# Kernel optimization log

Hardware: AMD Instinct MI355X
Metric: run time of the kernel (lower is better)

Reference implementation:

```python
import jax, jax.numpy as jnp
from jax import lax
import numpy as np

B, N, H, T, NPB = 1024, 50, 128, 50, 3
C_TANH, NEG = 10.0, 1e9


def _lstm(x, h, c, Wi, Wh, b):
    gates = x @ Wi + h @ Wh + b
    i, f, g, o = jnp.split(gates, 4, axis=-1)
    c2 = jax.nn.sigmoid(f) * c + jax.nn.sigmoid(i) * jnp.tanh(g)
    return jax.nn.sigmoid(o) * jnp.tanh(c2), c2


def setup_inputs() -> dict:
    key = jax.random.key(0)
    ks = jax.random.split(key, 20)
    rn = lambda k, shape, fan: (jax.random.normal(k, shape, jnp.float32) / np.float32(np.sqrt(fan)))
    return {
        'input_pnt': jax.random.uniform(ks[0], (B, N, 2), jnp.float32),
        'W_emb': rn(ks[1], (2, H), 2), 'b_emb': jnp.zeros((H,), jnp.float32),
        'dec_init': rn(ks[2], (1, 1, H), H),
        'Wi': rn(ks[3], (H, 4 * H), H), 'Wh': rn(ks[4], (H, 4 * H), H), 'b_lstm': jnp.zeros((4 * H,), jnp.float32),
        'Wq_g': rn(ks[5], (H, H), H), 'Wref_g': rn(ks[6], (H, H), H), 'v_g': rn(ks[7], (H,), H),
        'Wq_p': rn(ks[8], (H, H), H), 'Wref_p': rn(ks[9], (H, H), H), 'v_p': rn(ks[10], (H,), H),
        'Wi_c': rn(ks[11], (H, 4 * H), H), 'Wh_c': rn(ks[12], (H, 4 * H), H), 'b_c': jnp.zeros((4 * H,), jnp.float32),
        'Wq_c': rn(ks[13], (H, H), H), 'Wref_c': rn(ks[14], (H, H), H), 'v_c': rn(ks[15], (H,), H),
        'W1': rn(ks[16], (H, H), H), 'b1': jnp.zeros((H,), jnp.float32),
        'W2': rn(ks[17], (H, 1), H), 'b2': jnp.zeros((1,), jnp.float32),
    }


def _forward(input_pnt, W_emb, b_emb, dec_init, Wi, Wh, b_lstm, Wq_g, Wref_g, v_g,
             Wq_p, Wref_p, v_p, Wi_c, Wh_c, b_c, Wq_c, Wref_c, v_c, W1, b1, W2, b2):
    context = input_pnt @ W_emb + b_emb                    # [B,N,H] embedded nodes
    e_g = context @ Wref_g                                  # glimpse keys (step-invariant, hoisted)
    e_p = context @ Wref_p                                  # pointer keys (hoisted)
    z = jnp.zeros((B, H), context.dtype)
    carry0 = (z, z, jnp.zeros((B, N), context.dtype), jnp.broadcast_to(dec_init[0, 0], (B, H)))

    def step(carry, _):
        h, c, mask, dec_in = carry
        h2, c2 = _lstm(dec_in, h, c, Wi, Wh, b_lstm)
        # glimpse attention (masked)
        q = h2 @ Wq_g
        u = jnp.einsum('bnh,h->bn', jnp.tanh(e_g + q[:, None, :]), v_g) - NEG * mask
        g = jnp.einsum('bn,bnh->bh', jax.nn.softmax(u, -1), e_g)
        # pointer attention with tanh exploration clipping (masked)
        u2 = jnp.einsum('bnh,h->bn', jnp.tanh(e_p + (g @ Wq_p)[:, None, :]), v_p)
        logit = C_TANH * jnp.tanh(u2) - NEG * mask
        logprob = jax.nn.log_softmax(logit, -1)
        prob = jax.nn.softmax(logit, -1)
        action = jnp.argmax(prob, -1)                       # greedy decode
        mask2 = jnp.maximum(mask, jax.nn.one_hot(action, N, dtype=mask.dtype))
        dec_next = jnp.take_along_axis(context, action[:, None, None], axis=1)[:, 0]
        coords = jnp.take_along_axis(input_pnt, action[:, None, None], axis=1)[:, 0]
        return (h2, c2, mask2, dec_next), (logprob, prob, action, coords)

    (_, _, _, dec_last), (logprobs, probs, actions, coords) = lax.scan(step, carry0, None, length=T)
    logprobs = jnp.transpose(logprobs, (1, 0, 2))           # [B,T,N]
    probs = jnp.transpose(probs, (1, 0, 2))
    actions = jnp.transpose(actions, (1, 0))                # [B,T]
    coords = jnp.transpose(coords, (1, 0, 2))               # [B,T,2] visited coordinates
    # reward: TSP tour length
    seg = coords[:, 1:] - coords[:, :-1]
    close = coords[:, 0] - coords[:, -1]
    R = jnp.sum(jnp.sqrt(jnp.sum(seg * seg, -1) + 1e-10), -1) + jnp.sqrt(jnp.sum(close * close, -1) + 1e-10)
    # critic: one LSTM step on last action broadcast to hidden, cn[0], then process blocks
    a4c = jnp.broadcast_to(actions[:, -1].astype(context.dtype)[:, None], (B, H))
    _, hy = _lstm(a4c, z, z, Wi_c, Wh_c, b_c)
    enc = dec_last[:, None, :]                              # context gathered at last action, [B,1,H]
    e_c = enc @ Wref_c
    for _ in range(NPB):
        u = jnp.einsum('bnh,h->bn', jnp.tanh(e_c + (hy @ Wq_c)[:, None, :]), v_c)
        hy = jnp.einsum('bn,bnh->bh', jax.nn.softmax(C_TANH * jnp.tanh(u), -1), e_c)
    v = (jax.nn.relu(hy @ W1 + b1) @ W2 + b2)[:, 0]
    return R, v, logprobs, actions, coords, probs


def reference(input_pnt, W_emb, b_emb, dec_init, Wi, Wh, b_lstm, Wq_g, Wref_g, v_g,
              Wq_p, Wref_p, v_p, Wi_c, Wh_c, b_c, Wq_c, Wref_c, v_c, W1, b1, W2, b2):
    return _forward(input_pnt, W_emb, b_emb, dec_init, Wi, Wh, b_lstm, Wq_g, Wref_g, v_g,
                    Wq_p, Wref_p, v_p, Wi_c, Wh_c, b_c, Wq_c, Wref_c, v_c, W1, b1, W2, b2)
```

## Files before the change

### kernel.cpp

```cpp
#include <hip/hip_runtime.h>
#include <math.h>

#define Bsz 1024
#define Npt 50
#define Hd 128
#define G4 512
#define Tt 50
#define NEGC 1000000000.0f
#define CTANH 10.0f

#define OFF_R 0
#define OFF_V 1024
#define OFF_LP 2048
#define OFF_A 2562048
#define OFF_C 2613248
#define OFF_P 2715648

#define WS_TG 0
#define WS_TP 512
#define WS_TQ 1024
#define WS_A0 1536
#define WS_A1 2048
#define WS_A2 2560
#define WS_A3 3072
#define WS_CT 3584

__device__ __forceinline__ float fsig(float x) {
  return __builtin_amdgcn_rcpf(1.0f + __expf(-x));
}

__device__ __forceinline__ float ftanh(float x) {
  float e = __expf(2.0f * x);
  return 1.0f - 2.0f * __builtin_amdgcn_rcpf(e + 1.0f);
}

__device__ __forceinline__ float dpp_sum_bcast(float x) {
  int v;
  v = __builtin_amdgcn_update_dpp(0, __float_as_int(x), 0x111, 0xf, 0xf, true);
  x += __int_as_float(v);
  v = __builtin_amdgcn_update_dpp(0, __float_as_int(x), 0x112, 0xf, 0xf, true);
  x += __int_as_float(v);
  v = __builtin_amdgcn_update_dpp(0, __float_as_int(x), 0x114, 0xf, 0xf, true);
  x += __int_as_float(v);
  v = __builtin_amdgcn_update_dpp(0, __float_as_int(x), 0x118, 0xf, 0xf, true);
  x += __int_as_float(v);
  v = __builtin_amdgcn_update_dpp(0, __float_as_int(x), 0x142, 0xf, 0xf, true);
  x += __int_as_float(v);
  v = __builtin_amdgcn_update_dpp(0, __float_as_int(x), 0x143, 0xf, 0xf, true);
  x += __int_as_float(v);
  return __int_as_float(__builtin_amdgcn_readlane(__float_as_int(x), 63));
}

__device__ __forceinline__ float dpp_max_bcast(float x) {
  int v;
  v = __builtin_amdgcn_update_dpp(0, __float_as_int(x), 0x111, 0xf, 0xf, true);
  x = fmaxf(x, __int_as_float(v));
  v = __builtin_amdgcn_update_dpp(0, __float_as_int(x), 0x112, 0xf, 0xf, true);
  x = fmaxf(x, __int_as_float(v));
  v = __builtin_amdgcn_update_dpp(0, __float_as_int(x), 0x114, 0xf, 0xf, true);
  x = fmaxf(x, __int_as_float(v));
  v = __builtin_amdgcn_update_dpp(0, __float_as_int(x), 0x118, 0xf, 0xf, true);
  x = fmaxf(x, __int_as_float(v));
  v = __builtin_amdgcn_update_dpp(0, __float_as_int(x), 0x142, 0xf, 0xf, true);
  x = fmaxf(x, __int_as_float(v));
  v = __builtin_amdgcn_update_dpp(0, __float_as_int(x), 0x143, 0xf, 0xf, true);
  x = fmaxf(x, __int_as_float(v));
  return __int_as_float(__builtin_amdgcn_readlane(__float_as_int(x), 63));
}

__device__ __forceinline__ float xsum(float x) {
  #pragma unroll
  for (int off = 32; off >= 1; off >>= 1) x += __shfl_xor(x, off, 64);
  return x;
}

__global__ __launch_bounds__(512) void k_pre(const float* __restrict__ Wemb,
                                             const float* __restrict__ bemb,
                                             const float* __restrict__ dinit,
                                             const float* __restrict__ Wi,
                                             const float* __restrict__ bl,
                                             const float* __restrict__ Wqp,
                                             const float* __restrict__ Wrg,
                                             const float* __restrict__ Wrp,
                                             const float* __restrict__ vg,
                                             const float* __restrict__ vp,
                                             const float* __restrict__ Wrc,
                                             const float* __restrict__ W1,
                                             const float* __restrict__ b1,
                                             const float* __restrict__ W2,
                                             float* __restrict__ ws) {
  __shared__ float mg_s[2][128], mp_s[2][128], cg_s[128], cp_s[128];
  __shared__ float pg_s[2][128], pc_s[128];
  __shared__ float r0_s[128], r1_s[128], rc_s[128];
  int t = threadIdx.x;
  if (t < 256) {
    int j = t >> 7, hh = t & 127;
    float ag = 0.f, ap = 0.f;
    for (int k = 0; k < 128; ++k) {
      float we = Wemb[j * 128 + k];
      ag = fmaf(we, Wrg[k * 128 + hh], ag);
      ap = fmaf(we, Wrp[k * 128 + hh], ap);
    }
    mg_s[j][hh] = ag; mp_s[j][hh] = ap;
  } else if (t < 384) {
    int hh = t & 127;
    float cgv = 0.f, cpv = 0.f;
    for (int k = 0; k < 128; ++k) {
      float be = bemb[k];
      cgv = fmaf(be, Wrg[k * 128 + hh], cgv);
      cpv = fmaf(be, Wrp[k * 128 + hh], cpv);
    }
    cg_s[hh] = cgv; cp_s[hh] = cpv;
  } else {
    int hh = t & 127;
    float a0 = 0.f, a1 = 0.f, ac = 0.f;
    for (int k = 0; k < 128; ++k) {
      float wr = Wrc[k * 128 + hh];
      a0 = fmaf(Wemb[k], wr, a0);
      a1 = fmaf(Wemb[128 + k], wr, a1);
      ac = fmaf(bemb[k], wr, ac);
    }
    r0_s[hh] = a0; r1_s[hh] = a1; rc_s[hh] = ac;
  }
  __syncthreads();
  if (t < 256) {
    int j = t >> 7, hh = t & 127;
    float pg = 0.f;
    for (int k = 0; k < 128; ++k) pg = fmaf(mg_s[j][k], Wqp[k * 128 + hh], pg);
    pg_s[j][hh] = pg;
  } else if (t < 384) {
    int hh = t & 127;
    float pcv = 0.f;
    for (int k = 0; k < 128; ++k) pcv = fmaf(cg_s[k], Wqp[k * 128 + hh], pcv);
    pc_s[hh] = pcv + cp_s[hh];
  } else {
    int hh = t & 127;
    float t0 = 0.f, t1 = 0.f, tc = 0.f;
    for (int k = 0; k < 128; ++k) {
      float w1 = W1[k * 128 + hh];
      t0 = fmaf(r0_s[k], w1, t0);
      t1 = fmaf(r1_s[k], w1, t1);
      tc = fmaf(rc_s[k], w1, tc);
    }
    float4* w4 = (float4*)ws;
    w4[WS_CT / 4 + hh] = make_float4(t0, t1, tc + b1[hh], W2[hh]);
  }
  __syncthreads();
  if (t < 128) {
    float4* w4 = (float4*)ws;
    w4[WS_TG / 4 + t] = make_float4(mg_s[0][t], mg_s[1][t], vg[t], cg_s[t]);
    w4[WS_TP / 4 + t] = make_float4(mp_s[0][t], mp_s[1][t], vp[t], cp_s[t]);
    w4[WS_TQ / 4 + t] = make_float4(pg_s[0][t], pg_s[1][t], pc_s[t], 0.f);
  }
  {
    int j = t;
    float a0 = 0.f, a1 = 0.f, a2 = 0.f, a3 = 0.f;
    for (int k = 0; k < 128; ++k) {
      float wi = Wi[k * G4 + j];
      a0 = fmaf(Wemb[k], wi, a0);
      a1 = fmaf(Wemb[128 + k], wi, a1);
      a2 = fmaf(bemb[k], wi, a2);
      a3 = fmaf(dinit[k], wi, a3);
    }
    ws[WS_A0 + j] = a0;
    ws[WS_A1 + j] = a1;
    ws[WS_A2 + j] = a2 + bl[j];
    ws[WS_A3 + j] = a3 + bl[j];
  }
}

__global__ __launch_bounds__(1024, 4) void k_mega(const float* __restrict__ ip,
                                                  const float* __restrict__ Wh,
                                                  const float* __restrict__ Wqg,
                                                  const float* __restrict__ b2,
                                                  const float* __restrict__ ws,
                                                  float* __restrict__ out) {
  __shared__ __align__(16) float gpart[8][4][G4];
  __shared__ __align__(16) float qpart[8][4][Hd];
  __shared__ __align__(16) float up_s[4][4][64];
  __shared__ __align__(16) float up2_s[4][4][64];
  __shared__ __align__(16) float qc_s[4][Hd];
  __shared__ __align__(16) float h_s[4][Hd];
  __shared__ __align__(16) float c_s[4][Hd];
  __shared__ __align__(16) float tg_s[G4];
  __shared__ __align__(16) float tp_s[G4];
  __shared__ __align__(16) float tq_s[G4];
  __shared__ __align__(16) float ct_s[G4];
  __shared__ __align__(16) float a0_s[G4], a1_s[G4], a2_s[G4], a3_s[G4];
  __shared__ float vsum_s[2][4];
  __shared__ __align__(16) float ip_s[4][Npt * 2];
  __shared__ float mask_s[4][Npt];
  __shared__ float ch_s[4][Npt * 2];
  __shared__ float sel_s[4][2];
  __shared__ int ctr_s[4];

  int t = threadIdx.x, blk = blockIdx.x;
  int w = t >> 6, lane = t & 63;
  int kh = t >> 7, jt = t & 127;
  int k0q = kh * 16;

  float4 wv[16];
  #pragma unroll
  for (int j = 0; j < 16; ++j)
    wv[j] = *(const float4*)&Wh[(kh * 16 + j) * G4 + jt * 4];
  float wqr[16];
  #pragma unroll
  for (int j = 0; j < 16; ++j)
    wqr[j] = Wqg[(kh * 16 + j) * Hd + jt];

  const float4* ws4 = (const float4*)ws;
  if (t < 128) {
    float4 g4 = ws4[WS_TG / 4 + t];
    ((float4*)tg_s)[t] = make_float4(2.f * g4.x, 2.f * g4.y, -2.f * g4.z, 2.f * g4.w);
    float4 p4 = ws4[WS_TP / 4 + t];
    ((float4*)tp_s)[t] = make_float4(2.f * p4.x, 2.f * p4.y, -2.f * p4.z, 0.f);
    float4 q4 = ws4[WS_TQ / 4 + t];
    ((float4*)tq_s)[t] = make_float4(2.f * q4.x, 2.f * q4.y, 2.f * q4.z, 0.f);
    ((float4*)ct_s)[t] = ws4[WS_CT / 4 + t];
  } else if (t < 256) {
    int i = t - 128;
    ((float4*)a0_s)[i] = ((const float4*)(ws + WS_A0))[i];
    ((float4*)a1_s)[i] = ((const float4*)(ws + WS_A1))[i];
    ((float4*)a2_s)[i] = ((const float4*)(ws + WS_A2))[i];
    ((float4*)a3_s)[i] = ((const float4*)(ws + WS_A3))[i];
  }
  if (t < 200) {
    ((float2*)ip_s)[t] = ((const float2*)ip)[blk * 200 + t];
    ((float*)mask_s)[t] = 0.f;
  }
  if (t < 512) {
    int r = t >> 7, hh = t & 127;
    h_s[r][hh] = 0.f;
    c_s[r][hh] = 0.f;
  }
  if (t < 8) {
    int which = t >> 2, c = t & 3;
    float sv = 0.f;
    for (int hp = 0; hp < 32; ++hp)
      sv += ws[(which ? WS_TP : WS_TG) + (c * 32 + hp) * 4 + 2];
    vsum_s[which][c] = sv;
  }
  if (t < 8) ((float*)sel_s)[t] = 0.f;
  if (t < 4) ctr_s[t] = 0;
  {
    float4 z4 = make_float4(0.f, 0.f, 0.f, 0.f);
    #pragma unroll
    for (int i = 0; i < 4; ++i) ((float4*)gpart)[t * 4 + i] = z4;
  }
  __syncthreads();

  int cr = w & 3, hc = w >> 2;
  float2 pn = make_float2(0.f, 0.f);
  if (lane < Npt) pn = ((float2*)ip_s)[cr * Npt + lane];

  int lt = 0;
  auto lsync = [&]() {
    lt += 4;
    if (lane == 0)
      __hip_atomic_fetch_add(&ctr_s[cr], 1, __ATOMIC_RELEASE,
                             __HIP_MEMORY_SCOPE_WORKGROUP);
    while (__hip_atomic_load(&ctr_s[cr], __ATOMIC_ACQUIRE,
                             __HIP_MEMORY_SCOPE_WORKGROUP) < lt)
      __builtin_amdgcn_s_sleep(1);
  };

  auto A1row = [&](int r) {
    float hv[16];
    #pragma unroll
    for (int q4i = 0; q4i < 4; ++q4i)
      *(float4*)&hv[q4i * 4] = *(const float4*)&h_s[r][k0q + q4i * 4];
    float a0 = 0.f, a1 = 0.f, a2 = 0.f, a3 = 0.f;
    #pragma unroll
    for (int kk = 0; kk < 16; ++kk) {
      float4 wj = wv[kk];
      a0 = fmaf(hv[kk], wj.x, a0);
      a1 = fmaf(hv[kk], wj.y, a1);
      a2 = fmaf(hv[kk], wj.z, a2);
      a3 = fmaf(hv[kk], wj.w, a3);
    }
    *(float4*)&gpart[kh][r][jt * 4] = make_float4(a0, a1, a2, a3);
  };

  for (int s = 0; s < Tt; ++s) {
    __syncthreads();
    if (t < 512) {
      int r = t >> 7, hh = t & 127;
      float p0 = sel_s[r][0], p1 = sel_s[r][1];
      float g[4];
      #pragma unroll
      for (int gi = 0; gi < 4; ++gi) {
        int j = gi * 128 + hh;
        float x = (s == 0) ? a3_s[j]
                           : fmaf(p0, a0_s[j], fmaf(p1, a1_s[j], a2_s[j]));
        #pragma unroll
        for (int k8 = 0; k8 < 8; ++k8) x += gpart[k8][r][j];
        g[gi] = x;
      }
      float c2 = fsig(g[1]) * c_s[r][hh] + fsig(g[0]) * ftanh(g[2]);
      float h2 = fsig(g[3]) * ftanh(c2);
      c_s[r][hh] = c2;
      h_s[r][hh] = h2;
    }
    __syncthreads();
    {
      #pragma unroll
      for (int r = 0; r < 4; ++r) {
        float hv[16];
        #pragma unroll
        for (int q4i = 0; q4i < 4; ++q4i)
          *(float4*)&hv[q4i * 4] = *(const float4*)&h_s[r][k0q + q4i * 4];
        float a = 0.f;
        #pragma unroll
        for (int kk = 0; kk < 16; ++kk) a = fmaf(hv[kk], wqr[kk], a);
        qpart[kh][r][jt] = a;
      }
    }
    __syncthreads();
    if (s + 1 < Tt) {
      for (int r = 0; r < cr; ++r) A1row(r);
    }
    {
      if (lane < 32) {
        int h = hc * 32 + lane;
        float qs = ((float4*)tg_s)[h].w
                 + 2.f * (qpart[0][cr][h] + qpart[1][cr][h] + qpart[2][cr][h]
                        + qpart[3][cr][h] + qpart[4][cr][h] + qpart[5][cr][h]
                        + qpart[6][cr][h] + qpart[7][cr][h]);
        qc_s[cr][h] = qs;
      }
      float ac = vsum_s[0][hc];
      #pragma unroll 8
      for (int hp = 0; hp < 32; ++hp) {
        int h = hc * 32 + hp;
        float4 tg4 = ((float4*)tg_s)[h];
        float a = fmaf(pn.x, tg4.x, fmaf(pn.y, tg4.y, qc_s[cr][h]));
        ac = fmaf(tg4.z, __builtin_amdgcn_rcpf(__expf(a) + 1.0f), ac);
      }
      up_s[hc][cr][lane] = ac;
    }
    lsync();
    {
      float u = up_s[0][cr][lane] + up_s[1][cr][lane]
              + up_s[2][cr][lane] + up_s[3][cr][lane];
      float e = 0.f;
      if (lane < Npt) e = __expf(u - NEGC * mask_s[cr][lane]);
      float ssum = dpp_sum_bcast(e);
      float sx = dpp_sum_bcast(e * pn.x);
      float sy = dpp_sum_bcast(e * pn.y);
      float inv = __builtin_amdgcn_rcpf(ssum);
      float s0 = sx * inv;
      float s1 = sy * inv;
      if (lane < 32) {
        int h = hc * 32 + lane;
        float4 tq4 = ((float4*)tq_s)[h];
        qc_s[cr][h] = fmaf(s0, tq4.x, fmaf(s1, tq4.y, tq4.z));
      }
      float ac = vsum_s[1][hc];
      #pragma unroll 8
      for (int hp = 0; hp < 32; ++hp) {
        int h = hc * 32 + hp;
        float4 tp4 = ((float4*)tp_s)[h];
        float a = fmaf(pn.x, tp4.x, fmaf(pn.y, tp4.y, qc_s[cr][h]));
        ac = fmaf(tp4.z, __builtin_amdgcn_rcpf(__expf(a) + 1.0f), ac);
      }
      up2_s[hc][cr][lane] = ac;
    }
    lsync();
    if (hc == 3) {
      int row = cr, b = blk * 4 + row;
      float u = up2_s[0][row][lane] + up2_s[1][row][lane]
              + up2_s[2][row][lane] + up2_s[3][row][lane];
      float x = 0.f, e = 0.f;
      if (lane < Npt) {
        x = CTANH * ftanh(u) - NEGC * mask_s[row][lane];
        e = __expf(x);
      }
      float ssum = dpp_sum_bcast(e);
      float ls = __logf(ssum);
      float prob = e * __builtin_amdgcn_rcpf(ssum);
      if (lane < Npt) {
        out[OFF_LP + ((size_t)b * Tt + s) * Npt + lane] = x - ls;
        out[OFF_P + ((size_t)b * Tt + s) * Npt + lane] = prob;
      }
      float mx = dpp_max_bcast(prob);
      unsigned long long bal = __ballot((prob == mx) && (lane < Npt));
      int a = __ffsll(bal) - 1;
      float p0a = ip_s[row][2 * a];
      float p1a = ip_s[row][2 * a + 1];
      if (lane == 0) {
        out[OFF_A + (size_t)b * Tt + s] = (float)a;
        out[OFF_C + ((size_t)b * Tt + s) * 2 + 0] = p0a;
        out[OFF_C + ((size_t)b * Tt + s) * 2 + 1] = p1a;
        ((float2*)ch_s)[row * Npt + s] = make_float2(p0a, p1a);
        mask_s[row][a] = 1.0f;
        sel_s[row][0] = p0a;
        sel_s[row][1] = p1a;
      }
    }
    if (s + 1 < Tt) {
      for (int r = cr; r < 4; ++r) A1row(r);
    }
  }
  __syncthreads();

  if (w < 4) {
    int r = w, b = blk * 4 + r;
    float p0 = sel_s[r][0], p1 = sel_s[r][1];
    float4 ct0 = ((float4*)ct_s)[lane];
    float4 ct1 = ((float4*)ct_s)[64 + lane];
    float t1a = fmaxf(fmaf(p0, ct0.x, fmaf(p1, ct0.y, ct0.z)), 0.f);
    float t1b = fmaxf(fmaf(p0, ct1.x, fmaf(p1, ct1.y, ct1.z)), 0.f);
    float sv = xsum(t1a * ct0.w + t1b * ct1.w);
    if (lane == 0) out[OFF_V + b] = sv + b2[0];
    float rr = 0.f;
    if (lane < Npt) {
      float2 c0 = ((float2*)ch_s)[r * Npt + lane];
      float2 c1 = ((float2*)ch_s)[r * Npt + ((lane == Npt - 1) ? 0 : lane + 1)];
      float dx = c1.x - c0.x, dy = c1.y - c0.y;
      rr = sqrtf(dx * dx + dy * dy + 1e-10f);
    }
    rr = xsum(rr);
    if (lane == 0) out[OFF_R + b] = rr;
  }
}

extern "C" void kernel_launch(void* const* d_in, const int* in_sizes, int n_in,
                              void* d_out, int out_size, void* d_ws, size_t ws_size,
                              hipStream_t stream) {
  (void)in_sizes; (void)n_in; (void)out_size; (void)ws_size;
  const float* ip    = (const float*)d_in[0];
  const float* Wemb  = (const float*)d_in[1];
  const float* bemb  = (const float*)d_in[2];
  const float* dinit = (const float*)d_in[3];
  const float* Wi    = (const float*)d_in[4];
  const float* Wh    = (const float*)d_in[5];
  const float* bl    = (const float*)d_in[6];
  const float* Wqg   = (const float*)d_in[7];
  const float* Wrg   = (const float*)d_in[8];
  const float* vg    = (const float*)d_in[9];
  const float* Wqp   = (const float*)d_in[10];
  const float* Wrp   = (const float*)d_in[11];
  const float* vp    = (const float*)d_in[12];
  const float* Wrc   = (const float*)d_in[17];
  const float* W1    = (const float*)d_in[19];
  const float* b1    = (const float*)d_in[20];
  const float* W2    = (const float*)d_in[21];
  const float* b2    = (const float*)d_in[22];
  float* out = (float*)d_out;
  float* ws  = (float*)d_ws;

  k_pre<<<1, 512, 0, stream>>>(Wemb, bemb, dinit, Wi, bl, Wqp, Wrg, Wrp,
                               vg, vp, Wrc, W1, b1, W2, ws);
  k_mega<<<256, 1024, 0, stream>>>(ip, Wh, Wqg, b2, ws, out);
}
```

Before: 653.3 us.

## Compute recurrent LSTM gate matmul with split-bf16 MFMA instead of FP32 FMAs

Replaces the per-thread FP32 h@Wh partial sums, together with their 8-way LDS reduction buffer, with MFMA 16x16x32 bf16 instructions. Both operands are split into hi and lo bf16 parts (4 MFMAs per tile) to keep close to fp32 accuracy. Each of the 16 waves computes 32 gate columns, with four padded batch rows in a 16-row tile, and writes the results straight to gates_s. Separately, the glimpse and pointer query vectors are now broadcast with readlane instead of going through the qc_s shared buffer. This removes work that was previously spread across rows to overlap with attention, at the cost of 3/4 wasted MFMA rows and a conversion step each iteration.

```diff
diff --git a/kernel.cpp b/kernel.cpp
--- a/kernel.cpp
+++ b/kernel.cpp
@@ -25,6 +25,9 @@
 #define WS_A3 3072
 #define WS_CT 3584
 
+typedef __attribute__((ext_vector_type(8))) short s16x8;
+typedef __attribute__((ext_vector_type(4))) float fx4;
+
 __device__ __forceinline__ float fsig(float x) {
   return __builtin_amdgcn_rcpf(1.0f + __expf(-x));
 }
@@ -32,6 +35,15 @@
 __device__ __forceinline__ float ftanh(float x) {
   float e = __expf(2.0f * x);
   return 1.0f - 2.0f * __builtin_amdgcn_rcpf(e + 1.0f);
+}
+
+__device__ __forceinline__ unsigned short f2bf(float x) {
+  unsigned int u = __float_as_uint(x);
+  unsigned int r = (u + 0x7fffu + ((u >> 16) & 1u)) >> 16;
+  return (unsigned short)r;
+}
+__device__ __forceinline__ float bf2f(unsigned short b) {
+  return __uint_as_float(((unsigned int)b) << 16);
 }
 
 __device__ __forceinline__ float dpp_sum_bcast(float x) {
@@ -175,11 +187,11 @@
                                                   const float* __restrict__ b2,
                                                   const float* __restrict__ ws,
                                                   float* __restrict__ out) {
-  __shared__ __align__(16) float gpart[8][4][G4];
+  __shared__ __align__(16) float gates_s[4][G4];
+  __shared__ s16x8 afrag_s[4][2][64];
   __shared__ __align__(16) float qpart[8][4][Hd];
   __shared__ __align__(16) float up_s[4][4][64];
   __shared__ __align__(16) float up2_s[4][4][64];
-  __shared__ __align__(16) float qc_s[4][Hd];
   __shared__ __align__(16) float h_s[4][Hd];
   __shared__ __align__(16) float c_s[4][Hd];
   __shared__ __align__(16) float tg_s[G4];
@@ -199,10 +211,22 @@
   int kh = t >> 7, jt = t & 127;
   int k0q = kh * 16;
 
-  float4 wv[16];
-  #pragma unroll
-  for (int j = 0; j < 16; ++j)
-    wv[j] = *(const float4*)&Wh[(kh * 16 + j) * G4 + jt * 4];
+  s16x8 Bh[2][4], Bl[2][4];
+  {
+    int cb = (w << 5) + (lane & 15);
+    int g8 = (lane >> 4) << 3;
+    #pragma unroll
+    for (int tt = 0; tt < 2; ++tt)
+      #pragma unroll
+      for (int ks = 0; ks < 4; ++ks)
+        #pragma unroll
+        for (int j = 0; j < 8; ++j) {
+          float x = Wh[(size_t)((ks << 5) + g8 + j) * G4 + cb + (tt << 4)];
+          unsigned short hb = f2bf(x);
+          Bh[tt][ks][j] = (short)hb;
+          Bl[tt][ks][j] = (short)f2bf(x - bf2f(hb));
+        }
+  }
   float wqr[16];
   #pragma unroll
   for (int j = 0; j < 16; ++j)
@@ -233,6 +257,7 @@
     h_s[r][hh] = 0.f;
     c_s[r][hh] = 0.f;
   }
+  ((float2*)gates_s)[t] = make_float2(0.f, 0.f);
   if (t < 8) {
     int which = t >> 2, c = t & 3;
     float sv = 0.f;
@@ -242,11 +267,6 @@
   }
   if (t < 8) ((float*)sel_s)[t] = 0.f;
   if (t < 4) ctr_s[t] = 0;
-  {
-    float4 z4 = make_float4(0.f, 0.f, 0.f, 0.f);
-    #pragma unroll
-    for (int i = 0; i < 4; ++i) ((float4*)gpart)[t * 4 + i] = z4;
-  }
   __syncthreads();
 
   int cr = w & 3, hc = w >> 2;
@@ -262,23 +282,6 @@
     while (__hip_atomic_load(&ctr_s[cr], __ATOMIC_ACQUIRE,
                              __HIP_MEMORY_SCOPE_WORKGROUP) < lt)
       __builtin_amdgcn_s_sleep(1);
-  };
-
-  auto A1row = [&](int r) {
-    float hv[16];
-    #pragma unroll
-    for (int q4i = 0; q4i < 4; ++q4i)
-      *(float4*)&hv[q4i * 4] = *(const float4*)&h_s[r][k0q + q4i * 4];
-    float a0 = 0.f, a1 = 0.f, a2 = 0.f, a3 = 0.f;
-    #pragma unroll
-    for (int kk = 0; kk < 16; ++kk) {
-      float4 wj = wv[kk];
-      a0 = fmaf(hv[kk], wj.x, a0);
-      a1 = fmaf(hv[kk], wj.y, a1);
-      a2 = fmaf(hv[kk], wj.z, a2);
-      a3 = fmaf(hv[kk], wj.w, a3);
-    }
-    *(float4*)&gpart[kh][r][jt * 4] = make_float4(a0, a1, a2, a3);
   };
 
   for (int s = 0; s < Tt; ++s) {
@@ -292,9 +295,7 @@
         int j = gi * 128 + hh;
         float x = (s == 0) ? a3_s[j]
                            : fmaf(p0, a0_s[j], fmaf(p1, a1_s[j], a2_s[j]));
-        #pragma unroll
-        for (int k8 = 0; k8 < 8; ++k8) x += gpart[k8][r][j];
-        g[gi] = x;
+        g[gi] = x + gates_s[r][j];
       }
       float c2 = fsig(g[1]) * c_s[r][hh] + fsig(g[0]) * ftanh(g[2]);
       float h2 = fsig(g[3]) * ftanh(c2);
@@ -314,26 +315,46 @@
         for (int kk = 0; kk < 16; ++kk) a = fmaf(hv[kk], wqr[kk], a);
         qpart[kh][r][jt] = a;
       }
+      if (s + 1 < Tt && w >= 8 && w < 12) {
+        int ks = w - 8, row = lane & 15, g8 = (lane >> 4) << 3;
+        float xv[8];
+        if (row < 4) {
+          const float* hp8 = &h_s[row][(ks << 5) + g8];
+          *(float4*)&xv[0] = *(const float4*)hp8;
+          *(float4*)&xv[4] = *(const float4*)(hp8 + 4);
+        } else {
+          #pragma unroll
+          for (int j = 0; j < 8; ++j) xv[j] = 0.f;
+        }
+        s16x8 hf, lf;
+        #pragma unroll
+        for (int j = 0; j < 8; ++j) {
+          unsigned short hb = f2bf(xv[j]);
+          hf[j] = (short)hb;
+          lf[j] = (short)f2bf(xv[j] - bf2f(hb));
+        }
+        afrag_s[ks][0][lane] = hf;
+        afrag_s[ks][1][lane] = lf;
+      }
     }
     __syncthreads();
-    if (s + 1 < Tt) {
-      for (int r = 0; r < cr; ++r) A1row(r);
-    }
     {
+      float qs = 0.f;
       if (lane < 32) {
         int h = hc * 32 + lane;
-        float qs = ((float4*)tg_s)[h].w
-                 + 2.f * (qpart[0][cr][h] + qpart[1][cr][h] + qpart[2][cr][h]
-                        + qpart[3][cr][h] + qpart[4][cr][h] + qpart[5][cr][h]
-                        + qpart[6][cr][h] + qpart[7][cr][h]);
-        qc_s[cr][h] = qs;
-      }
+        qs = ((float4*)tg_s)[h].w
+           + 2.f * (qpart[0][cr][h] + qpart[1][cr][h] + qpart[2][cr][h]
+                  + qpart[3][cr][h] + qpart[4][cr][h] + qpart[5][cr][h]
+                  + qpart[6][cr][h] + qpart[7][cr][h]);
+      }
+      int qsb = __float_as_int(qs);
       float ac = vsum_s[0][hc];
       #pragma unroll 8
       for (int hp = 0; hp < 32; ++hp) {
         int h = hc * 32 + hp;
         float4 tg4 = ((float4*)tg_s)[h];
-        float a = fmaf(pn.x, tg4.x, fmaf(pn.y, tg4.y, qc_s[cr][h]));
+        float qv = __int_as_float(__builtin_amdgcn_readlane(qsb, hp));
+        float a = fmaf(pn.x, tg4.x, fmaf(pn.y, tg4.y, qv));
         ac = fmaf(tg4.z, __builtin_amdgcn_rcpf(__expf(a) + 1.0f), ac);
       }
       up_s[hc][cr][lane] = ac;
@@ -350,17 +371,20 @@
       float inv = __builtin_amdgcn_rcpf(ssum);
       float s0 = sx * inv;
       float s1 = sy * inv;
+      float qs2 = 0.f;
       if (lane < 32) {
         int h = hc * 32 + lane;
         float4 tq4 = ((float4*)tq_s)[h];
-        qc_s[cr][h] = fmaf(s0, tq4.x, fmaf(s1, tq4.y, tq4.z));
-      }
+        qs2 = fmaf(s0, tq4.x, fmaf(s1, tq4.y, tq4.z));
+      }
+      int q2b = __float_as_int(qs2);
       float ac = vsum_s[1][hc];
       #pragma unroll 8
       for (int hp = 0; hp < 32; ++hp) {
         int h = hc * 32 + hp;
         float4 tp4 = ((float4*)tp_s)[h];
-        float a = fmaf(pn.x, tp4.x, fmaf(pn.y, tp4.y, qc_s[cr][h]));
+        float qv = __int_as_float(__builtin_amdgcn_readlane(q2b, hp));
+        float a = fmaf(pn.x, tp4.x, fmaf(pn.y, tp4.y, qv));
         ac = fmaf(tp4.z, __builtin_amdgcn_rcpf(__expf(a) + 1.0f), ac);
       }
       up2_s[hc][cr][lane] = ac;
@@ -398,7 +422,28 @@
       }
     }
     if (s + 1 < Tt) {
-      for (int r = cr; r < 4; ++r) A1row(r);
+      fx4 d0 = {0.f, 0.f, 0.f, 0.f}, d1 = {0.f, 0.f, 0.f, 0.f};
+      #pragma unroll
+      for (int ks = 0; ks < 4; ++ks) {
+        s16x8 ah = afrag_s[ks][0][lane];
+        s16x8 al = afrag_s[ks][1][lane];
+        d0 = __builtin_amdgcn_mfma_f32_16x16x32_bf16(ah, Bh[0][ks], d0, 0, 0, 0);
+        d0 = __builtin_amdgcn_mfma_f32_16x16x32_bf16(ah, Bl[0][ks], d0, 0, 0, 0);
+        d0 = __builtin_amdgcn_mfma_f32_16x16x32_bf16(al, Bh[0][ks], d0, 0, 0, 0);
+        d0 = __builtin_amdgcn_mfma_f32_16x16x32_bf16(al, Bl[0][ks], d0, 0, 0, 0);
+        d1 = __builtin_amdgcn_mfma_f32_16x16x32_bf16(ah, Bh[1][ks], d1, 0, 0, 0);
+        d1 = __builtin_amdgcn_mfma_f32_16x16x32_bf16(ah, Bl[1][ks], d1, 0, 0, 0);
+        d1 = __builtin_amdgcn_mfma_f32_16x16x32_bf16(al, Bh[1][ks], d1, 0, 0, 0);
+        d1 = __builtin_amdgcn_mfma_f32_16x16x32_bf16(al, Bl[1][ks], d1, 0, 0, 0);
+      }
+      if (lane < 16) {
+        int c0 = (w << 5) + lane;
+        #pragma unroll
+        for (int rr = 0; rr < 4; ++rr) {
+          gates_s[rr][c0] = d0[rr];
+          gates_s[rr][c0 + 16] = d1[rr];
+        }
+      }
     }
   }
   __syncthreads();
```

Measured after the change: 623.7 us. 4.5% less time.
